# Kernel optimization log

Measured on AMD Instinct MI355X. Metric: run time of the kernel, lower is better.

The kernel has to match this reference:

```python
import jax, jax.numpy as jnp
import numpy as np
from jax.ops import segment_sum

N_NODES = 200_000
N_EDGES = 6_400_000


def gcn_conv(x, W, b, src, dst, num_nodes):
    """PyG GCNConv (default): h = x @ W; add self-loops; symmetric norm; scatter-add; + bias."""
    h = x @ W  # [N, F_out]
    loop = jnp.arange(num_nodes, dtype=src.dtype)
    s = jnp.concatenate([src, loop])  # source (message sender)
    d = jnp.concatenate([dst, loop])  # target (aggregation index)
    ones = jnp.ones(s.shape[0], dtype=h.dtype)
    deg = segment_sum(ones, d, num_segments=num_nodes)  # in-degree incl. self-loop
    dinv = jnp.where(deg > 0, jax.lax.rsqrt(deg), 0.0)
    norm = dinv[s] * dinv[d]  # [E+N]
    msg = h[s] * norm[:, None]  # [E+N, F_out]
    out = segment_sum(msg, d, num_segments=num_nodes)
    return out + b


def setup_inputs() -> dict:
    key = jax.random.key(0)
    ks = jax.random.split(key, 6)
    x = jax.random.normal(ks[0], (N_NODES, 6), dtype=jnp.float32)
    edge_index = jax.random.randint(ks[1], (2, N_EDGES), 0, N_NODES, dtype=jnp.int32)
    W1 = jax.random.normal(ks[2], (6, 16), dtype=jnp.float32) * (1.0 / np.sqrt(6))
    b1 = jnp.zeros((16,), dtype=jnp.float32)
    W2 = jax.random.normal(ks[3], (16, 8), dtype=jnp.float32) * (1.0 / np.sqrt(16))
    b2 = jnp.zeros((8,), dtype=jnp.float32)
    Wfc = jax.random.normal(ks[4], (8, 1), dtype=jnp.float32) * (1.0 / np.sqrt(8))
    bfc = jnp.zeros((1,), dtype=jnp.float32)
    return {"x": x, "edge_index": edge_index, "W1": W1, "b1": b1,
            "W2": W2, "b2": b2, "Wfc": Wfc, "bfc": bfc}


def reference(x, edge_index, W1, b1, W2, b2, Wfc, bfc):
    src, dst = edge_index[0], edge_index[1]
    h = gcn_conv(x, W1, b1, src, dst, N_NODES)
    h = jax.nn.relu(h)
    h = gcn_conv(h, W2, b2, src, dst, N_NODES)
    h = jax.nn.relu(h)
    out = h @ Wfc + bfc
    return jax.nn.sigmoid(out)
```

## Files before the change

### kernel.cpp

```cpp
#include <hip/hip_runtime.h>
#include <math.h>


#define TPB 256
#define NBS 8
#define NBKT 256
#define MAXB 1024
#define BPT (MAXB / TPB)
#define CHUNK 4096
#define EPT (CHUNK / TPB)
#define CAP 9216
#define RPT (CAP / TPB)
#define NWAVE (TPB / 64)
#define NSEG 32

__device__ __forceinline__ unsigned short f2bf(float f) {
    unsigned u = __float_as_uint(f);
    unsigned r = (u + 0x7FFFu + ((u >> 16) & 1u)) >> 16;
    return (unsigned short)r;
}
__device__ __forceinline__ unsigned pk2(float a, float b) {
    return (unsigned)f2bf(a) | ((unsigned)f2bf(b) << 16);
}
#define BFLO(u) __uint_as_float((u) << 16)
#define BFHI(u) __uint_as_float((u) & 0xFFFF0000u)

__global__ void __launch_bounds__(TPB) k_fb1(
        const int* __restrict__ dst, int* __restrict__ C, int e, int nb) {
    __shared__ int h[MAXB];
    int t = threadIdx.x;
    int c0 = blockIdx.x * CHUNK;
    int csize = min(e - c0, CHUNK);
#pragma unroll
    for (int k = 0; k < BPT; k++) h[t * BPT + k] = 0;
    __syncthreads();
    if (csize == CHUNK && ((((size_t)(const void*)(dst + c0)) & 15) == 0)) {
        const int4* d4 = (const int4*)(dst + c0);
#pragma unroll
        for (int k = 0; k < EPT / 4; k++) {
            int4 d = d4[t + k * TPB];
            atomicAdd(&h[d.x >> NBS], 1);
            atomicAdd(&h[d.y >> NBS], 1);
            atomicAdd(&h[d.z >> NBS], 1);
            atomicAdd(&h[d.w >> NBS], 1);
        }
    } else {
        for (int i = t; i < csize; i += TPB)
            atomicAdd(&h[dst[c0 + i] >> NBS], 1);
    }
    __syncthreads();
    int* row = C + (size_t)blockIdx.x * nb;
    for (int b = t; b < nb; b += TPB) row[b] = h[b];
}

__global__ void __launch_bounds__(TPB) k_scan1(
        const int* __restrict__ C, int* __restrict__ O, int* __restrict__ Sseg,
        int nchunk, int nb, int cps, int ngrp) {
    int bid = blockIdx.x;
    int s = bid / ngrp, g = bid - s * ngrp;
    int b = g * TPB + threadIdx.x;
    if (b >= nb) return;
    int cbeg = s * cps;
    int cend = min(cbeg + cps, nchunk);
    int run = 0;
#pragma unroll 4
    for (int c = cbeg; c < cend; c++) {
        int v = C[(size_t)c * nb + b];
        O[(size_t)c * nb + b] = run;
        run += v;
    }
    Sseg[s * nb + b] = run;
}

__global__ void __launch_bounds__(TPB) k_scan2(
        const int* __restrict__ Sseg, int* __restrict__ segbase,
        int* __restrict__ btot, int nb) {
    int b = blockIdx.x * TPB + threadIdx.x;
    if (b >= nb) return;
    int run = b * CAP;
#pragma unroll
    for (int s = 0; s < NSEG; s++) {
        segbase[s * nb + b] = run;
        run += Sseg[s * nb + b];
    }
    btot[b] = run - b * CAP;
}

__global__ void __launch_bounds__(TPB) k_fillbin(
        const int* __restrict__ src, const int* __restrict__ dst,
        const int* __restrict__ O, const int* __restrict__ segbase,
        int* __restrict__ binned, int e, int nb, int cps) {
    __shared__ int stage[CHUNK];
    __shared__ unsigned short bs[CHUNK];
    __shared__ int h[MAXB];
    __shared__ int delta[MAXB];
    __shared__ int wsum[NWAVE];
    int t = threadIdx.x;
    int c0 = blockIdx.x * CHUNK;
    int csize = min(e - c0, CHUNK);
#pragma unroll
    for (int k = 0; k < BPT; k++) h[t * BPT + k] = 0;
    __syncthreads();
    int dreg[EPT], sreg[EPT];
    if (csize == CHUNK && ((((size_t)(const void*)(dst + c0)) & 15) == 0)
                       && ((((size_t)(const void*)(src + c0)) & 15) == 0)) {
        const int4* d4 = (const int4*)(dst + c0);
        const int4* s4 = (const int4*)(src + c0);
#pragma unroll
        for (int k = 0; k < EPT / 4; k++) {
            int4 d = d4[t + k * TPB];
            int4 s = s4[t + k * TPB];
            dreg[4 * k + 0] = d.x; sreg[4 * k + 0] = s.x;
            dreg[4 * k + 1] = d.y; sreg[4 * k + 1] = s.y;
            dreg[4 * k + 2] = d.z; sreg[4 * k + 2] = s.z;
            dreg[4 * k + 3] = d.w; sreg[4 * k + 3] = s.w;
            atomicAdd(&h[d.x >> NBS], 1);
            atomicAdd(&h[d.y >> NBS], 1);
            atomicAdd(&h[d.z >> NBS], 1);
            atomicAdd(&h[d.w >> NBS], 1);
        }
    } else {
#pragma unroll
        for (int k = 0; k < EPT; k++) {
            int idx = t + k * TPB;
            int d = (idx < csize) ? dst[c0 + idx] : -1;
            int s = (idx < csize) ? src[c0 + idx] : 0;
            dreg[k] = d;
            sreg[k] = s;
            if (d >= 0) atomicAdd(&h[d >> NBS], 1);
        }
    }
    __syncthreads();
    int loc[BPT], hreg[BPT];
    int ts = 0;
#pragma unroll
    for (int k = 0; k < BPT; k++) {
        hreg[k] = h[t * BPT + k];
        loc[k] = ts;
        ts += hreg[k];
    }
    int lane = t & 63, wid = t >> 6;
    int v = ts;
#pragma unroll
    for (int off = 1; off < 64; off <<= 1) {
        int u = __shfl_up(v, off);
        if (lane >= off) v += u;
    }
    if (lane == 63) wsum[wid] = v;
    __syncthreads();
    int pre = 0;
#pragma unroll
    for (int wq = 0; wq < NWAVE - 1; wq++)
        if (wid > wq) pre += wsum[wq];
    int tbase = pre + v - ts;
    const int* Orow = O + (size_t)blockIdx.x * nb;
    const int* segrow = segbase + (size_t)(blockIdx.x / cps) * nb;
#pragma unroll
    for (int k = 0; k < BPT; k++) {
        int b = t * BPT + k;
        int ex = tbase + loc[k];
        h[b] = ex;
        delta[b] = (b < nb) ? (segrow[b] + Orow[b] - ex) : 0;
    }
    __syncthreads();
#pragma unroll
    for (int k = 0; k < EPT; k++) {
        int d = dreg[k];
        if (d >= 0) {
            int b = d >> NBS;
            int r = atomicAdd(&h[b], 1);
            stage[r] = ((d & (NBKT - 1)) << 18) | sreg[k];
            bs[r] = (unsigned short)b;
        }
    }
    __syncthreads();
    for (int k = t; k < csize; k += TPB)
        binned[delta[bs[k]] + k] = stage[k];
}

__global__ void __launch_bounds__(TPB) k_sort(
        const int* __restrict__ binned, const int* __restrict__ btot,
        const float* __restrict__ x, int* __restrict__ csr,
        int* __restrict__ rowptr, int* __restrict__ rowend,
        float* __restrict__ dinv, uint4* __restrict__ xdq, int n) {
    __shared__ int stage[CAP];
    __shared__ int cnt[NBKT];
    __shared__ int curs[NBKT];
    __shared__ int wsum[NWAVE];
    int b = blockIdx.x, t = threadIdx.x;
    int base = b * CAP;
    int c = btot[b];
    cnt[t] = 0;
    __syncthreads();
    int w[RPT];
#pragma unroll
    for (int k = 0; k < RPT; k++) {
        int idx = t + k * TPB;
        w[k] = (idx < c) ? binned[base + idx] : -1;
        if (w[k] >= 0) atomicAdd(&cnt[w[k] >> 18], 1);
    }
    __syncthreads();
    int v = cnt[t];
    int lane = t & 63, wid = t >> 6;
    int iv = v;
#pragma unroll
    for (int off = 1; off < 64; off <<= 1) {
        int u = __shfl_up(iv, off);
        if (lane >= off) iv += u;
    }
    if (lane == 63) wsum[wid] = iv;
    __syncthreads();
    int pre = 0;
#pragma unroll
    for (int wq = 0; wq < NWAVE - 1; wq++)
        if (wid > wq) pre += wsum[wq];
    int ex = pre + iv - v;
    curs[t] = ex;
    int i = (b << NBS) + t;
    rowptr[i] = base + ex;
    rowend[i] = base + ex + v;
    if (i < n) {
        float di = rsqrtf((float)(v + 1));
        dinv[i] = di;
        uint4 q;
        q.x = pk2(x[i * 6 + 0] * di, x[i * 6 + 1] * di);
        q.y = pk2(x[i * 6 + 2] * di, x[i * 6 + 3] * di);
        q.z = pk2(x[i * 6 + 4] * di, x[i * 6 + 5] * di);
        q.w = 0;
        xdq[i] = q;
    }
    __syncthreads();
#pragma unroll
    for (int k = 0; k < RPT; k++) {
        if (w[k] >= 0) {
            int r = atomicAdd(&curs[w[k] >> 18], 1);
            stage[r] = w[k] & 0x3FFFF;
        }
    }
    __syncthreads();
    for (int k = t; k < c; k += TPB)
        csr[base + k] = stage[k];
}

__global__ void __launch_bounds__(TPB) k_gat1(
        const uint4* __restrict__ xdq, const int* __restrict__ csr,
        const int* __restrict__ rowptr, const int* __restrict__ rowend,
        const float* __restrict__ dinv,
        const float* __restrict__ b1, const float* __restrict__ W1,
        const float* __restrict__ W2, uint2* __restrict__ g2q, int n) {
    __shared__ float w1[96];
    __shared__ float w2[128];
    __shared__ float bb[16];
    if (threadIdx.x < 96) w1[threadIdx.x] = W1[threadIdx.x];
    if (threadIdx.x < 128) w2[threadIdx.x] = W2[threadIdx.x];
    if (threadIdx.x < 16) bb[threadIdx.x] = b1[threadIdx.x];
    __syncthreads();
    int sub = threadIdx.x & 15;
    int i = blockIdx.x * 16 + (threadIdx.x >> 4);
    bool valid = (i < n);
    int r0 = rowptr[i], r1 = rowend[i];
    float a0 = 0.f, a1 = 0.f, a2 = 0.f, a3 = 0.f, a4 = 0.f, a5 = 0.f;
    float c0 = 0.f, c1 = 0.f, c2 = 0.f, c3 = 0.f, c4 = 0.f, c5 = 0.f;
    if (valid && sub == 0) {
        uint4 q = xdq[i];
        a0 += BFLO(q.x); a1 += BFHI(q.x);
        a2 += BFLO(q.y); a3 += BFHI(q.y);
        a4 += BFLO(q.z); a5 += BFHI(q.z);
    }
    int j = r0 + sub;
    while (j + 16 < r1) {
        uint4 q = xdq[csr[j]];
        uint4 p = xdq[csr[j + 16]];
        a0 += BFLO(q.x); a1 += BFHI(q.x);
        a2 += BFLO(q.y); a3 += BFHI(q.y);
        a4 += BFLO(q.z); a5 += BFHI(q.z);
        c0 += BFLO(p.x); c1 += BFHI(p.x);
        c2 += BFLO(p.y); c3 += BFHI(p.y);
        c4 += BFLO(p.z); c5 += BFHI(p.z);
        j += 32;
    }
    if (j < r1) {
        uint4 q = xdq[csr[j]];
        a0 += BFLO(q.x); a1 += BFHI(q.x);
        a2 += BFLO(q.y); a3 += BFHI(q.y);
        a4 += BFLO(q.z); a5 += BFHI(q.z);
    }
    a0 += c0; a1 += c1; a2 += c2; a3 += c3; a4 += c4; a5 += c5;
#pragma unroll
    for (int m = 1; m <= 8; m <<= 1) {
        a0 += __shfl_xor(a0, m); a1 += __shfl_xor(a1, m);
        a2 += __shfl_xor(a2, m); a3 += __shfl_xor(a3, m);
        a4 += __shfl_xor(a4, m); a5 += __shfl_xor(a5, m);
    }
    float di = valid ? dinv[i] : 0.f;
    int f = sub;
    float hf = a0 * w1[f] + a1 * w1[16 + f] + a2 * w1[32 + f]
             + a3 * w1[48 + f] + a4 * w1[64 + f] + a5 * w1[80 + f];
    float tf = fmaxf(di * hf + bb[f], 0.0f);
    float p0 = tf * w2[f * 8 + 0], p1 = tf * w2[f * 8 + 1];
    float p2 = tf * w2[f * 8 + 2], p3 = tf * w2[f * 8 + 3];
    float p4 = tf * w2[f * 8 + 4], p5 = tf * w2[f * 8 + 5];
    float p6 = tf * w2[f * 8 + 6], p7 = tf * w2[f * 8 + 7];
#pragma unroll
    for (int m = 1; m <= 8; m <<= 1) {
        p0 += __shfl_xor(p0, m); p1 += __shfl_xor(p1, m);
        p2 += __shfl_xor(p2, m); p3 += __shfl_xor(p3, m);
        p4 += __shfl_xor(p4, m); p5 += __shfl_xor(p5, m);
        p6 += __shfl_xor(p6, m); p7 += __shfl_xor(p7, m);
    }
    if (valid && sub < 2) {
        float q0 = sub ? p4 : p0, q1 = sub ? p5 : p1;
        float q2 = sub ? p6 : p2, q3 = sub ? p7 : p3;
        uint2 o;
        o.x = pk2(q0 * di, q1 * di);
        o.y = pk2(q2 * di, q3 * di);
        g2q[i * 2 + sub] = o;
    }
}

__global__ void __launch_bounds__(TPB) k_gat2(
        const uint4* __restrict__ g2q, const int* __restrict__ csr,
        const int* __restrict__ rowptr, const int* __restrict__ rowend,
        const float* __restrict__ dinv,
        const float* __restrict__ b2, const float* __restrict__ Wfc,
        const float* __restrict__ bfc, float* __restrict__ out, int n) {
    __shared__ float w[8];
    __shared__ float bb[8];
    __shared__ float bf;
    if (threadIdx.x < 8) { w[threadIdx.x] = Wfc[threadIdx.x]; bb[threadIdx.x] = b2[threadIdx.x]; }
    if (threadIdx.x == 0) bf = bfc[0];
    __syncthreads();
    int sub = threadIdx.x & 15;
    int i = blockIdx.x * 16 + (threadIdx.x >> 4);
    bool valid = (i < n);
    int r0 = rowptr[i], r1 = rowend[i];
    float a0 = 0.f, a1 = 0.f, a2 = 0.f, a3 = 0.f;
    float a4 = 0.f, a5 = 0.f, a6 = 0.f, a7 = 0.f;
    if (valid && sub == 0) {
        uint4 q = g2q[i];
        a0 += BFLO(q.x); a1 += BFHI(q.x); a2 += BFLO(q.y); a3 += BFHI(q.y);
        a4 += BFLO(q.z); a5 += BFHI(q.z); a6 += BFLO(q.w); a7 += BFHI(q.w);
    }
    float c0 = 0.f, c1 = 0.f, c2 = 0.f, c3 = 0.f;
    float c4 = 0.f, c5 = 0.f, c6 = 0.f, c7 = 0.f;
    int j = r0 + sub;
    while (j + 16 < r1) {
        uint4 q = g2q[csr[j]];
        uint4 p = g2q[csr[j + 16]];
        a0 += BFLO(q.x); a1 += BFHI(q.x); a2 += BFLO(q.y); a3 += BFHI(q.y);
        a4 += BFLO(q.z); a5 += BFHI(q.z); a6 += BFLO(q.w); a7 += BFHI(q.w);
        c0 += BFLO(p.x); c1 += BFHI(p.x); c2 += BFLO(p.y); c3 += BFHI(p.y);
        c4 += BFLO(p.z); c5 += BFHI(p.z); c6 += BFLO(p.w); c7 += BFHI(p.w);
        j += 32;
    }
    if (j < r1) {
        uint4 q = g2q[csr[j]];
        a0 += BFLO(q.x); a1 += BFHI(q.x); a2 += BFLO(q.y); a3 += BFHI(q.y);
        a4 += BFLO(q.z); a5 += BFHI(q.z); a6 += BFLO(q.w); a7 += BFHI(q.w);
    }
    a0 += c0; a1 += c1; a2 += c2; a3 += c3;
    a4 += c4; a5 += c5; a6 += c6; a7 += c7;
#pragma unroll
    for (int m = 1; m <= 8; m <<= 1) {
        a0 += __shfl_xor(a0, m); a1 += __shfl_xor(a1, m);
        a2 += __shfl_xor(a2, m); a3 += __shfl_xor(a3, m);
        a4 += __shfl_xor(a4, m); a5 += __shfl_xor(a5, m);
        a6 += __shfl_xor(a6, m); a7 += __shfl_xor(a7, m);
    }
    if (valid && sub == 0) {
        float di = dinv[i];
        float o = bf;
        o += fmaxf(di * a0 + bb[0], 0.0f) * w[0];
        o += fmaxf(di * a1 + bb[1], 0.0f) * w[1];
        o += fmaxf(di * a2 + bb[2], 0.0f) * w[2];
        o += fmaxf(di * a3 + bb[3], 0.0f) * w[3];
        o += fmaxf(di * a4 + bb[4], 0.0f) * w[4];
        o += fmaxf(di * a5 + bb[5], 0.0f) * w[5];
        o += fmaxf(di * a6 + bb[6], 0.0f) * w[6];
        o += fmaxf(di * a7 + bb[7], 0.0f) * w[7];
        out[i] = 1.0f / (1.0f + expf(-o));
    }
}

extern "C" void kernel_launch(void* const* d_in, const int* in_sizes, int n_in,
                              void* d_out, int out_size, void* d_ws, size_t ws_size,
                              hipStream_t stream) {
    const float* x   = (const float*)d_in[0];
    const int*   ei  = (const int*)d_in[1];
    const float* W1  = (const float*)d_in[2];
    const float* b1  = (const float*)d_in[3];
    const float* W2  = (const float*)d_in[4];
    const float* b2  = (const float*)d_in[5];
    const float* Wfc = (const float*)d_in[6];
    const float* bfc = (const float*)d_in[7];
    float* out = (float*)d_out;

    const int n = in_sizes[0] / 6;
    const int e = in_sizes[1] / 2;
    const int* src = ei;
    const int* dst = ei + e;
    const int nb = (n + NBKT - 1) >> NBS;
    const size_t np = (size_t)nb << NBS;
    const int nblk = (e + CHUNK - 1) / CHUNK;
    const int cps = (nblk + NSEG - 1) / NSEG;
    const int ngrp = (nb + TPB - 1) / TPB;
    const size_t reg = (size_t)nb * CAP;

    int* C       = (int*)d_ws;
    int* O       = C + (size_t)nblk * nb;
    int* Sseg    = O + (size_t)nblk * nb;
    int* segbase = Sseg + (size_t)NSEG * MAXB;
    int* btot    = segbase + (size_t)NSEG * MAXB;
    int* binned  = btot + MAXB;
    int* csr     = binned + reg;
    int* rowptr  = csr + reg;
    int* rowend  = rowptr + np;
    float* dinv  = (float*)(rowend + np);
    uint4* xdq   = (uint4*)(dinv + np);
    uint2* g2q   = (uint2*)(xdq + np);

    int gw = (n + 15) / 16;

    k_fb1<<<nblk, TPB, 0, stream>>>(dst, C, e, nb);
    k_scan1<<<NSEG * ngrp, TPB, 0, stream>>>(C, O, Sseg, nblk, nb, cps, ngrp);
    k_scan2<<<ngrp, TPB, 0, stream>>>(Sseg, segbase, btot, nb);
    k_fillbin<<<nblk, TPB, 0, stream>>>(src, dst, O, segbase, binned, e, nb, cps);
    k_sort<<<nb, TPB, 0, stream>>>(binned, btot, x, csr, rowptr, rowend, dinv, xdq, n);
    k_gat1<<<gw, TPB, 0, stream>>>(xdq, csr, rowptr, rowend, dinv, b1, W1, W2, g2q, n);
    k_gat2<<<gw, TPB, 0, stream>>>((const uint4*)g2q, csr, rowptr, rowend, dinv, b2, Wfc, bfc, out, n);
}
```

Baseline: 244.6 us.

## Fuse first-layer gather into bucket sort using global degree histogram

Computes per-node in-degree with global atomics in the first histogram pass, and a new small kernel uses it to build dinv and the bf16 scaled features before sorting. The first GCN layer's aggregation and both weight transforms are then done inside the bucket-sort kernel, one thread per node, reading neighbour indices straight from shared-memory staging. This removes the separate layer-1 gather kernel and its csr/rowptr reads. In exchange it adds 6.4M global atomics on deg, and the per-thread serial neighbour loop leaves each node's work to a single thread, with load imbalance across threads.

```diff
diff --git a/kernel.cpp b/kernel.cpp
--- a/kernel.cpp
+++ b/kernel.cpp
@@ -26,7 +26,8 @@
 #define BFHI(u) __uint_as_float((u) & 0xFFFF0000u)
 
 __global__ void __launch_bounds__(TPB) k_fb1(
-        const int* __restrict__ dst, int* __restrict__ C, int e, int nb) {
+        const int* __restrict__ dst, int* __restrict__ C,
+        int* __restrict__ deg, int e, int nb) {
     __shared__ int h[MAXB];
     int t = threadIdx.x;
     int c0 = blockIdx.x * CHUNK;
@@ -43,10 +44,17 @@
             atomicAdd(&h[d.y >> NBS], 1);
             atomicAdd(&h[d.z >> NBS], 1);
             atomicAdd(&h[d.w >> NBS], 1);
+            atomicAdd(&deg[d.x], 1);
+            atomicAdd(&deg[d.y], 1);
+            atomicAdd(&deg[d.z], 1);
+            atomicAdd(&deg[d.w], 1);
         }
     } else {
-        for (int i = t; i < csize; i += TPB)
-            atomicAdd(&h[dst[c0 + i] >> NBS], 1);
+        for (int i = t; i < csize; i += TPB) {
+            int d = dst[c0 + i];
+            atomicAdd(&h[d >> NBS], 1);
+            atomicAdd(&deg[d], 1);
+        }
     }
     __syncthreads();
     int* row = C + (size_t)blockIdx.x * nb;
@@ -86,6 +94,21 @@
     btot[b] = run - b * CAP;
 }
 
+__global__ void __launch_bounds__(TPB) k_prep(
+        const int* __restrict__ deg, const float* __restrict__ x,
+        float* __restrict__ dinv, uint4* __restrict__ xdq, int n) {
+    int i = blockIdx.x * TPB + threadIdx.x;
+    if (i >= n) return;
+    float di = rsqrtf((float)(deg[i] + 1));
+    dinv[i] = di;
+    uint4 q;
+    q.x = pk2(x[i * 6 + 0] * di, x[i * 6 + 1] * di);
+    q.y = pk2(x[i * 6 + 2] * di, x[i * 6 + 3] * di);
+    q.z = pk2(x[i * 6 + 4] * di, x[i * 6 + 5] * di);
+    q.w = 0;
+    xdq[i] = q;
+}
+
 __global__ void __launch_bounds__(TPB) k_fillbin(
         const int* __restrict__ src, const int* __restrict__ dst,
         const int* __restrict__ O, const int* __restrict__ segbase,
@@ -180,14 +203,22 @@
 
 __global__ void __launch_bounds__(TPB) k_sort(
         const int* __restrict__ binned, const int* __restrict__ btot,
-        const float* __restrict__ x, int* __restrict__ csr,
+        const uint4* __restrict__ xdq, const float* __restrict__ dinv,
+        const float* __restrict__ b1, const float* __restrict__ W1,
+        const float* __restrict__ W2, int* __restrict__ csr,
         int* __restrict__ rowptr, int* __restrict__ rowend,
-        float* __restrict__ dinv, uint4* __restrict__ xdq, int n) {
+        uint4* __restrict__ g2q, int n) {
     __shared__ int stage[CAP];
     __shared__ int cnt[NBKT];
     __shared__ int curs[NBKT];
     __shared__ int wsum[NWAVE];
+    __shared__ float w1[96];
+    __shared__ float w2[128];
+    __shared__ float bb[16];
     int b = blockIdx.x, t = threadIdx.x;
+    if (t < 96) w1[t] = W1[t];
+    if (t < 128) w2[t] = W2[t];
+    if (t < 16) bb[t] = b1[t];
     int base = b * CAP;
     int c = btot[b];
     cnt[t] = 0;
@@ -219,16 +250,6 @@
     int i = (b << NBS) + t;
     rowptr[i] = base + ex;
     rowend[i] = base + ex + v;
-    if (i < n) {
-        float di = rsqrtf((float)(v + 1));
-        dinv[i] = di;
-        uint4 q;
-        q.x = pk2(x[i * 6 + 0] * di, x[i * 6 + 1] * di);
-        q.y = pk2(x[i * 6 + 2] * di, x[i * 6 + 3] * di);
-        q.z = pk2(x[i * 6 + 4] * di, x[i * 6 + 5] * di);
-        q.w = 0;
-        xdq[i] = q;
-    }
     __syncthreads();
 #pragma unroll
     for (int k = 0; k < RPT; k++) {
@@ -240,81 +261,51 @@
     __syncthreads();
     for (int k = t; k < c; k += TPB)
         csr[base + k] = stage[k];
-}
-
-__global__ void __launch_bounds__(TPB) k_gat1(
-        const uint4* __restrict__ xdq, const int* __restrict__ csr,
-        const int* __restrict__ rowptr, const int* __restrict__ rowend,
-        const float* __restrict__ dinv,
-        const float* __restrict__ b1, const float* __restrict__ W1,
-        const float* __restrict__ W2, uint2* __restrict__ g2q, int n) {
-    __shared__ float w1[96];
-    __shared__ float w2[128];
-    __shared__ float bb[16];
-    if (threadIdx.x < 96) w1[threadIdx.x] = W1[threadIdx.x];
-    if (threadIdx.x < 128) w2[threadIdx.x] = W2[threadIdx.x];
-    if (threadIdx.x < 16) bb[threadIdx.x] = b1[threadIdx.x];
-    __syncthreads();
-    int sub = threadIdx.x & 15;
-    int i = blockIdx.x * 16 + (threadIdx.x >> 4);
-    bool valid = (i < n);
-    int r0 = rowptr[i], r1 = rowend[i];
     float a0 = 0.f, a1 = 0.f, a2 = 0.f, a3 = 0.f, a4 = 0.f, a5 = 0.f;
-    float c0 = 0.f, c1 = 0.f, c2 = 0.f, c3 = 0.f, c4 = 0.f, c5 = 0.f;
-    if (valid && sub == 0) {
+    if (i < n) {
         uint4 q = xdq[i];
+        a0 = BFLO(q.x); a1 = BFHI(q.x);
+        a2 = BFLO(q.y); a3 = BFHI(q.y);
+        a4 = BFLO(q.z); a5 = BFHI(q.z);
+    }
+    int kk = ex, kend = ex + v;
+    for (; kk + 4 <= kend; kk += 4) {
+        int s0 = stage[kk], s1 = stage[kk + 1];
+        int s2 = stage[kk + 2], s3 = stage[kk + 3];
+        uint4 q0 = xdq[s0], q1 = xdq[s1], q2 = xdq[s2], q3 = xdq[s3];
+        a0 += BFLO(q0.x) + BFLO(q1.x) + BFLO(q2.x) + BFLO(q3.x);
+        a1 += BFHI(q0.x) + BFHI(q1.x) + BFHI(q2.x) + BFHI(q3.x);
+        a2 += BFLO(q0.y) + BFLO(q1.y) + BFLO(q2.y) + BFLO(q3.y);
+        a3 += BFHI(q0.y) + BFHI(q1.y) + BFHI(q2.y) + BFHI(q3.y);
+        a4 += BFLO(q0.z) + BFLO(q1.z) + BFLO(q2.z) + BFLO(q3.z);
+        a5 += BFHI(q0.z) + BFHI(q1.z) + BFHI(q2.z) + BFHI(q3.z);
+    }
+    for (; kk < kend; kk++) {
+        uint4 q = xdq[stage[kk]];
         a0 += BFLO(q.x); a1 += BFHI(q.x);
         a2 += BFLO(q.y); a3 += BFHI(q.y);
         a4 += BFLO(q.z); a5 += BFHI(q.z);
     }
-    int j = r0 + sub;
-    while (j + 16 < r1) {
-        uint4 q = xdq[csr[j]];
-        uint4 p = xdq[csr[j + 16]];
-        a0 += BFLO(q.x); a1 += BFHI(q.x);
-        a2 += BFLO(q.y); a3 += BFHI(q.y);
-        a4 += BFLO(q.z); a5 += BFHI(q.z);
-        c0 += BFLO(p.x); c1 += BFHI(p.x);
-        c2 += BFLO(p.y); c3 += BFHI(p.y);
-        c4 += BFLO(p.z); c5 += BFHI(p.z);
-        j += 32;
-    }
-    if (j < r1) {
-        uint4 q = xdq[csr[j]];
-        a0 += BFLO(q.x); a1 += BFHI(q.x);
-        a2 += BFLO(q.y); a3 += BFHI(q.y);
-        a4 += BFLO(q.z); a5 += BFHI(q.z);
-    }
-    a0 += c0; a1 += c1; a2 += c2; a3 += c3; a4 += c4; a5 += c5;
-#pragma unroll
-    for (int m = 1; m <= 8; m <<= 1) {
-        a0 += __shfl_xor(a0, m); a1 += __shfl_xor(a1, m);
-        a2 += __shfl_xor(a2, m); a3 += __shfl_xor(a3, m);
-        a4 += __shfl_xor(a4, m); a5 += __shfl_xor(a5, m);
-    }
-    float di = valid ? dinv[i] : 0.f;
-    int f = sub;
-    float hf = a0 * w1[f] + a1 * w1[16 + f] + a2 * w1[32 + f]
-             + a3 * w1[48 + f] + a4 * w1[64 + f] + a5 * w1[80 + f];
-    float tf = fmaxf(di * hf + bb[f], 0.0f);
-    float p0 = tf * w2[f * 8 + 0], p1 = tf * w2[f * 8 + 1];
-    float p2 = tf * w2[f * 8 + 2], p3 = tf * w2[f * 8 + 3];
-    float p4 = tf * w2[f * 8 + 4], p5 = tf * w2[f * 8 + 5];
-    float p6 = tf * w2[f * 8 + 6], p7 = tf * w2[f * 8 + 7];
-#pragma unroll
-    for (int m = 1; m <= 8; m <<= 1) {
-        p0 += __shfl_xor(p0, m); p1 += __shfl_xor(p1, m);
-        p2 += __shfl_xor(p2, m); p3 += __shfl_xor(p3, m);
-        p4 += __shfl_xor(p4, m); p5 += __shfl_xor(p5, m);
-        p6 += __shfl_xor(p6, m); p7 += __shfl_xor(p7, m);
-    }
-    if (valid && sub < 2) {
-        float q0 = sub ? p4 : p0, q1 = sub ? p5 : p1;
-        float q2 = sub ? p6 : p2, q3 = sub ? p7 : p3;
-        uint2 o;
-        o.x = pk2(q0 * di, q1 * di);
-        o.y = pk2(q2 * di, q3 * di);
-        g2q[i * 2 + sub] = o;
+    if (i < n) {
+        float di = dinv[i];
+        float o0 = 0.f, o1 = 0.f, o2 = 0.f, o3 = 0.f;
+        float o4 = 0.f, o5 = 0.f, o6 = 0.f, o7 = 0.f;
+#pragma unroll
+        for (int f = 0; f < 16; f++) {
+            float hf = a0 * w1[f] + a1 * w1[16 + f] + a2 * w1[32 + f]
+                     + a3 * w1[48 + f] + a4 * w1[64 + f] + a5 * w1[80 + f];
+            float tf = fmaxf(di * hf + bb[f], 0.0f);
+            o0 += tf * w2[f * 8 + 0]; o1 += tf * w2[f * 8 + 1];
+            o2 += tf * w2[f * 8 + 2]; o3 += tf * w2[f * 8 + 3];
+            o4 += tf * w2[f * 8 + 4]; o5 += tf * w2[f * 8 + 5];
+            o6 += tf * w2[f * 8 + 6]; o7 += tf * w2[f * 8 + 7];
+        }
+        uint4 r;
+        r.x = pk2(o0 * di, o1 * di);
+        r.y = pk2(o2 * di, o3 * di);
+        r.z = pk2(o4 * di, o5 * di);
+        r.w = pk2(o6 * di, o7 * di);
+        g2q[i] = r;
     }
 }
 
@@ -411,21 +402,26 @@
     int* Sseg    = O + (size_t)nblk * nb;
     int* segbase = Sseg + (size_t)NSEG * MAXB;
     int* btot    = segbase + (size_t)NSEG * MAXB;
-    int* binned  = btot + MAXB;
+    int* deg     = btot + MAXB;
+    int* binned  = deg + np;
     int* csr     = binned + reg;
     int* rowptr  = csr + reg;
     int* rowend  = rowptr + np;
     float* dinv  = (float*)(rowend + np);
-    uint4* xdq   = (uint4*)(dinv + np);
-    uint2* g2q   = (uint2*)(xdq + np);
+    size_t off   = (size_t)((int*)(dinv + np) - (int*)d_ws);
+    off = (off + 3) & ~(size_t)3;
+    uint4* xdq   = (uint4*)((int*)d_ws + off);
+    uint4* g2q   = xdq + np;
 
     int gw = (n + 15) / 16;
 
-    k_fb1<<<nblk, TPB, 0, stream>>>(dst, C, e, nb);
+    hipMemsetAsync(deg, 0, np * sizeof(int), stream);
+    k_fb1<<<nblk, TPB, 0, stream>>>(dst, C, deg, e, nb);
     k_scan1<<<NSEG * ngrp, TPB, 0, stream>>>(C, O, Sseg, nblk, nb, cps, ngrp);
     k_scan2<<<ngrp, TPB, 0, stream>>>(Sseg, segbase, btot, nb);
+    k_prep<<<(n + TPB - 1) / TPB, TPB, 0, stream>>>(deg, x, dinv, xdq, n);
     k_fillbin<<<nblk, TPB, 0, stream>>>(src, dst, O, segbase, binned, e, nb, cps);
-    k_sort<<<nb, TPB, 0, stream>>>(binned, btot, x, csr, rowptr, rowend, dinv, xdq, n);
-    k_gat1<<<gw, TPB, 0, stream>>>(xdq, csr, rowptr, rowend, dinv, b1, W1, W2, g2q, n);
-    k_gat2<<<gw, TPB, 0, stream>>>((const uint4*)g2q, csr, rowptr, rowend, dinv, b2, Wfc, bfc, out, n);
-}
+    k_sort<<<nb, TPB, 0, stream>>>(binned, btot, xdq, dinv, b1, W1, W2,
+                                   csr, rowptr, rowend, g2q, n);
+    k_gat2<<<gw, TPB, 0, stream>>>(g2q, csr, rowptr, rowend, dinv, b2, Wfc, bfc, out, n);
+}
```

Measured after the change: 491.2 us. 101% more time.
